# Kernel tuning notes

Hardware: AMD Instinct MI355X
Metric: run time of the kernel (lower is better)

The kernel has to match this reference:

```python
import jax, jax.numpy as jnp
import numpy as np

D = 512
DB = D // 4          # 128
R = 4                # window radius
KB = 9               # boundary kernel
DH = D // 2          # attn mlp hidden
VOCABS = {"quality": 64, "root": 13, "bass": 13, "key": 25}
COMPS = ["quality", "root", "bass", "key"]
B, T = 4, 4096


def _ln(x, g, b, eps=1e-5):
    mu = jnp.mean(x, axis=-1, keepdims=True)
    var = jnp.var(x, axis=-1, keepdims=True)
    return (x - mu) * jax.lax.rsqrt(var + eps) * g + b


def setup_inputs() -> dict:
    key = jax.random.key(0)
    ks = jax.random.split(key, 24)
    s = 0.02
    inp = {
        "h": jax.random.normal(ks[0], (B, T, D), jnp.float32),
        # boundary head
        "w_bnd": jax.random.normal(ks[1], (D,), jnp.float32) * s,
        "b_bnd": jnp.zeros((1,), jnp.float32),
        # boundary smoother conv1d(1,1,KB)
        "conv_k": jax.random.normal(ks[2], (KB,), jnp.float32) * s,
        "conv_b": jnp.zeros((1,), jnp.float32),
        # FiLM boundary embeddings
        "e0": jnp.zeros((DB,), jnp.float32),
        "e1": jax.random.normal(ks[3], (DB,), jnp.float32) * s,
        # LayerNorms
        "ln_in_g": jnp.ones((D + DB,), jnp.float32),
        "ln_in_b": jnp.zeros((D + DB,), jnp.float32),
        "ln_h_g": jnp.ones((D,), jnp.float32),
        "ln_h_b": jnp.zeros((D,), jnp.float32),
        # FiLM mlp
        "film_w": jax.random.normal(ks[4], (D + DB, 2 * D), jnp.float32) * s,
        "film_b": jnp.zeros((2 * D,), jnp.float32),
        # per-component attn MLP (stacked over 4 comps)
        "attn_w1": jax.random.normal(ks[5], (4, D, DH), jnp.float32) * s,
        "attn_b1": jnp.zeros((4, DH), jnp.float32),
        "attn_w2": jax.random.normal(ks[6], (4, DH), jnp.float32) * s,
        "attn_b2": jnp.zeros((4,), jnp.float32),
        # per-component projector first layer (stacked)
        "proj_w1": jax.random.normal(ks[7], (4, D, D), jnp.float32) * s,
        "proj_b1": jnp.zeros((4, D), jnp.float32),
    }
    for i, c in enumerate(COMPS):
        inp[f"proj_w2_{c[0]}" if c != "key" else "proj_w2_k"] = jax.random.normal(ks[8 + i], (D, VOCABS[c]), jnp.float32) * s
        inp[f"proj_b2_{c[0]}" if c != "key" else "proj_b2_k"] = jnp.zeros((VOCABS[c],), jnp.float32)
    return inp


def reference(h, w_bnd, b_bnd, conv_k, conv_b, e0, e1,
              ln_in_g, ln_in_b, ln_h_g, ln_h_b, film_w, film_b,
              attn_w1, attn_b1, attn_w2, attn_b2, proj_w1, proj_b1,
              proj_w2_q, proj_b2_q, proj_w2_r, proj_b2_r,
              proj_w2_b, proj_b2_b, proj_w2_k, proj_b2_k):
    Bz, Tz, Dz = h.shape
    # boundary head + smoothing (conv1d, same padding) + sigmoid
    bl = jnp.einsum("btd,d->bt", h, w_bnd) + b_bnd[0]            # [B,T]
    sm = jax.lax.conv_general_dilated(bl[:, None, :], conv_k[None, None, :],
                                      (1,), [(KB // 2, KB // 2)]) + conv_b[0]
    b_soft = jax.nn.sigmoid(sm[:, 0, :])                          # [B,T]
    # FiLM
    eb = b_soft[..., None] * e1 + (1.0 - b_soft[..., None]) * e0  # [B,T,DB]
    film_in = _ln(jnp.concatenate([h, eb], axis=-1), ln_in_g, ln_in_b)
    gb = film_in @ film_w + film_b                                # [B,T,2D]
    gamma, beta = gb[..., :Dz], gb[..., Dz:]
    z = _ln(h, ln_h_g, ln_h_b) * (1.0 + gamma) + beta             # [B,T,D]
    # local windows via replicate pad + gather
    hp = jnp.pad(h, ((0, 0), (R, R), (0, 0)), mode="edge")        # [B,T+2R,D]
    idx = jnp.arange(Tz)[:, None] + jnp.arange(2 * R + 1)[None, :]  # [T,W]
    local = hp[:, idx, :]                                         # [B,T,W,D]
    c = jnp.concatenate([z[:, :, None, :], local], axis=2)        # [B,T,C,D]
    # attention pooling for all 4 components at once
    s1 = jax.nn.gelu(jnp.einsum("btcd,kdh->kbtch", c, attn_w1)
                     + attn_b1[:, None, None, None, :], approximate=False)
    scores = jnp.einsum("kbtch,kh->kbtc", s1, attn_w2) + attn_b2[:, None, None, None]
    attn = jax.nn.softmax(scores, axis=-1)                        # [K,B,T,C]
    pooled = jnp.einsum("kbtc,btcd->kbtd", attn, c)               # [K,B,T,D]
    p1 = jax.nn.gelu(jnp.einsum("kbtd,kde->kbte", pooled, proj_w1)
                     + proj_b1[:, None, None, :], approximate=False)
    lq = p1[0] @ proj_w2_q + proj_b2_q
    lr = p1[1] @ proj_w2_r + proj_b2_r
    lb = p1[2] @ proj_w2_b + proj_b2_b
    lk = p1[3] @ proj_w2_k + proj_b2_k
    return jnp.concatenate([lq, lr, lb, lk, bl[..., None]], axis=-1)  # [B,T,116]
```

## Files before the change

kernel.cpp:

```cpp
#include <hip/hip_runtime.h>
#include <hip/hip_bf16.h>

typedef unsigned short u16;
typedef unsigned int u32;

#define NR 16384
#define TT 4096

typedef __bf16 bf16_t;
typedef bf16_t bf16x8 __attribute__((ext_vector_type(8)));
typedef float f32x4 __attribute__((ext_vector_type(4)));

__device__ __forceinline__ float b2f(u16 u){ return __uint_as_float(((u32)u)<<16); }
__device__ __forceinline__ u16 f2b(float f){
  u32 u = __float_as_uint(f);
  u32 r = u + 0x7fffu + ((u>>16)&1u);
  return (u16)(r>>16);
}
__device__ __forceinline__ void up2(u32 u, float&a, float&b){
  a = __uint_as_float(u<<16);
  b = __uint_as_float(u & 0xffff0000u);
}
__device__ __forceinline__ void ld8(const u16* p, float* f){
  uint4 v = *(const uint4*)p;
  up2(v.x,f[0],f[1]); up2(v.y,f[2],f[3]);
  up2(v.z,f[4],f[5]); up2(v.w,f[6],f[7]);
}
__device__ __forceinline__ float wred(float v){
  #pragma unroll
  for(int o=32;o>0;o>>=1) v += __shfl_down(v,o,64);
  return v;
}
__device__ __forceinline__ float gelu_f(float x){
  float x2 = x*x;
  float u = x*(0.7978845608f + 0.0356774081f*x2);
  float e = __expf(2.0f*u);
  float t = 1.0f - 2.0f*__builtin_amdgcn_rcpf(e+1.0f);
  return 0.5f*x*(1.0f+t);
}
__device__ __forceinline__ void gl_lds(const void* g, void* l){
  __builtin_amdgcn_global_load_lds(
      (__attribute__((address_space(1))) void*)(void*)g,
      (__attribute__((address_space(3))) void*)l, 16, 0, 0);
}

__global__ void k_tw(const float* __restrict__ src, u16* __restrict__ dst,
                     int K, int N, long long sS, long long sD){
  __shared__ float t[32][33];
  const float* S = src + (size_t)blockIdx.z*sS;
  u16* D = dst + (size_t)blockIdx.z*sD;
  int k0 = blockIdx.y*32, n0 = blockIdx.x*32;
  int r = threadIdx.x>>5, c = threadIdx.x&31;
  #pragma unroll
  for(int p=0;p<4;p++) t[r+p*8][c] = S[(size_t)(k0+r+p*8)*N + n0 + c];
  __syncthreads();
  #pragma unroll
  for(int p=0;p<4;p++) D[(size_t)(n0+r+p*8)*K + k0 + c] = f2b(t[c][r+p*8]);
}

__global__ void k_w2c(const float* __restrict__ wq, const float* __restrict__ bq,
                      const float* __restrict__ wr, const float* __restrict__ br,
                      const float* __restrict__ wb_, const float* __restrict__ bb_,
                      const float* __restrict__ wk, const float* __restrict__ bk,
                      u16* __restrict__ W2c, float* __restrict__ b2c){
  int idx = blockIdx.x;
  int p = idx>>5, j = idx&31, tid = threadIdx.x;
  const float* Wm; const float* Bm; int V; int cofs = 0;
  if(p<=1){ Wm=wq; Bm=bq; V=64; cofs = p*32; }
  else if(p==2){ Wm=wr; Bm=br; V=13; }
  else if(p==3){ Wm=wb_; Bm=bb_; V=13; }
  else { Wm=wk; Bm=bk; V=25; }
  int c = j + cofs;
  bool valid = c < V;
  for(int k=tid;k<512;k+=256)
    W2c[(size_t)idx*512 + k] = f2b(valid ? Wm[(size_t)k*V + c] : 0.f);
  if(tid==0) b2c[idx] = valid ? Bm[c] : 0.f;
}

__global__ void k_bnd(const float* __restrict__ h, const float* __restrict__ wb,
                      const float* __restrict__ bb,
                      float* __restrict__ bl, float* __restrict__ hsum, float* __restrict__ hss,
                      u16* __restrict__ hbf, float* __restrict__ out){
  int wave = threadIdx.x>>6, lane = threadIdx.x&63;
  int n = blockIdx.x*4 + wave;
  const float4* hp = (const float4*)(h + (size_t)n*512 + lane*8);
  const float4* wp = (const float4*)(wb + lane*8);
  float4 h0 = hp[0], h1 = hp[1], w0 = wp[0], w1 = wp[1];
  float hv[8] = {h0.x,h0.y,h0.z,h0.w,h1.x,h1.y,h1.z,h1.w};
  float wv[8] = {w0.x,w0.y,w0.z,w0.w,w1.x,w1.y,w1.z,w1.w};
  float dot=0.f, s=0.f, ss=0.f;
  #pragma unroll
  for(int i=0;i<8;i++){ dot += hv[i]*wv[i]; s += hv[i]; ss += hv[i]*hv[i]; }
  u16* hd = hbf + (size_t)n*512 + lane*8;
  *(ushort4*)hd     = make_ushort4(f2b(hv[0]),f2b(hv[1]),f2b(hv[2]),f2b(hv[3]));
  *(ushort4*)(hd+4) = make_ushort4(f2b(hv[4]),f2b(hv[5]),f2b(hv[6]),f2b(hv[7]));
  dot = wred(dot); s = wred(s); ss = wred(ss);
  if(lane==0){
    float v = dot + bb[0];
    bl[n] = v; hsum[n]=s; hss[n]=ss;
    out[(size_t)n*116 + 115] = v;
  }
}

__global__ void k_conv(const float* __restrict__ bl, const float* __restrict__ ck,
                       const float* __restrict__ cb, float* __restrict__ bsoft){
  int n = blockIdx.x*256 + threadIdx.x;
  int b = n>>12, t = n&4095;
  float acc = cb[0];
  #pragma unroll
  for(int i=0;i<9;i++){
    int tt = t-4+i;
    if(tt>=0 && tt<TT) acc += bl[(b<<12)+tt]*ck[i];
  }
  bsoft[n] = 1.0f/(1.0f+expf(-acc));
}

__global__ void k_filmin(const float* __restrict__ h, const float* __restrict__ bsoft,
                         const float* __restrict__ e0, const float* __restrict__ e1,
                         const float* __restrict__ g, const float* __restrict__ bb,
                         u16* __restrict__ fin){
  __shared__ float xb[640];
  __shared__ float red[8];
  int n = blockIdx.x, tid = threadIdx.x;
  float bs = bsoft[n];
  float s=0.f, ss=0.f;
  for(int idx=tid; idx<640; idx+=256){
    float v;
    if(idx<512) v = h[(size_t)n*512+idx];
    else { int j=idx-512; v = bs*e1[j] + (1.0f-bs)*e0[j]; }
    xb[idx]=v; s+=v; ss+=v*v;
  }
  s = wred(s); ss = wred(ss);
  int wave = tid>>6, lane = tid&63;
  if(lane==0){ red[wave]=s; red[wave+4]=ss; }
  __syncthreads();
  float S = red[0]+red[1]+red[2]+red[3];
  float SS = red[4]+red[5]+red[6]+red[7];
  float mu = S*(1.0f/640.0f);
  float var = SS*(1.0f/640.0f) - mu*mu;
  float rs = rsqrtf(var + 1e-5f);
  for(int idx=tid; idx<640; idx+=256){
    float v = (xb[idx]-mu)*rs*g[idx] + bb[idx];
    fin[(size_t)n*640+idx] = f2b(v);
  }
}

__global__ __launch_bounds__(256) void k_film(
    const u16* __restrict__ fin, const u16* __restrict__ WT, const float* __restrict__ fbias,
    const float* __restrict__ hsum, const float* __restrict__ hss,
    const float* __restrict__ lng, const float* __restrict__ lnb,
    const u16* __restrict__ hbf, u16* __restrict__ z){
  __shared__ __align__(16) u16 As[128*32];
  __shared__ __align__(16) u16 Bg[128*32];
  __shared__ __align__(16) u16 Bb2[128*32];
  int tid = threadIdx.x, wave = tid>>6, lane = tid&63;
  int cg0 = blockIdx.x*128, row0 = blockIdx.y*128;
  int wr = (wave>>1)*64, wc = (wave&1)*64;
  int lrow = lane>>2, lcol = (lane&3)*8, m15 = lane&15, q = lane>>4;
  f32x4 ag[4][4] = {}, ab[4][4] = {};
  for(int k0=0;k0<640;k0+=32){
    const u16* ga = fin + (size_t)(row0 + wave*32 + lrow)*640 + k0 + lcol;
    u16* la = As + wave*32*32;
    gl_lds(ga, la); gl_lds(ga + (size_t)16*640, la + 16*32);
    const u16* gg = WT + (size_t)(cg0 + wave*32 + lrow)*640 + k0 + lcol;
    u16* lg = Bg + wave*32*32;
    gl_lds(gg, lg); gl_lds(gg + (size_t)16*640, lg + 16*32);
    const u16* gb2 = WT + (size_t)(cg0 + 512 + wave*32 + lrow)*640 + k0 + lcol;
    u16* lb2 = Bb2 + wave*32*32;
    gl_lds(gb2, lb2); gl_lds(gb2 + (size_t)16*640, lb2 + 16*32);
    __syncthreads();
    bf16x8 af[4], bg[4], bb[4];
    #pragma unroll
    for(int i=0;i<4;i++){
      af[i] = *(const bf16x8*)&As[(wr + i*16 + m15)*32 + q*8];
      bg[i] = *(const bf16x8*)&Bg[(wc + i*16 + m15)*32 + q*8];
      bb[i] = *(const bf16x8*)&Bb2[(wc + i*16 + m15)*32 + q*8];
    }
    #pragma unroll
    for(int i=0;i<4;i++)
      #pragma unroll
      for(int j=0;j<4;j++){
        ag[i][j] = __builtin_amdgcn_mfma_f32_16x16x32_bf16(bg[j], af[i], ag[i][j], 0,0,0);
        ab[i][j] = __builtin_amdgcn_mfma_f32_16x16x32_bf16(bb[j], af[i], ab[i][j], 0,0,0);
      }
    __syncthreads();
  }
  #pragma unroll
  for(int i=0;i<4;i++){
    int m = row0 + wr + i*16 + m15;
    float mu = hsum[m]*(1.0f/512.0f);
    float var = hss[m]*(1.0f/512.0f) - mu*mu;
    float rs = rsqrtf(var + 1e-5f);
    #pragma unroll
    for(int j=0;j<4;j++){
      int d0 = cg0 + wc + j*16 + q*4;
      float4 g4 = *(const float4*)&lng[d0];
      float4 b4 = *(const float4*)&lnb[d0];
      float4 fg = *(const float4*)&fbias[d0];
      float4 fb = *(const float4*)&fbias[512+d0];
      float hv[4];
      { ushort4 hb4 = *(const ushort4*)(hbf + (size_t)m*512 + d0);
        hv[0]=b2f(hb4.x); hv[1]=b2f(hb4.y); hv[2]=b2f(hb4.z); hv[3]=b2f(hb4.w); }
      float gm[4] = {ag[i][j][0]+fg.x, ag[i][j][1]+fg.y, ag[i][j][2]+fg.z, ag[i][j][3]+fg.w};
      float bt[4] = {ab[i][j][0]+fb.x, ab[i][j][1]+fb.y, ab[i][j][2]+fb.z, ab[i][j][3]+fb.w};
      float gg4[4] = {g4.x,g4.y,g4.z,g4.w}, bb4[4] = {b4.x,b4.y,b4.z,b4.w};
      u16 o[4];
      #pragma unroll
      for(int r=0;r<4;r++){
        float ln = (hv[r]-mu)*rs*gg4[r] + bb4[r];
        o[r] = f2b(ln*(1.0f+gm[r]) + bt[r]);
      }
      *(ushort4*)(z + (size_t)m*512 + d0) = make_ushort4(o[0],o[1],o[2],o[3]);
    }
  }
}

__global__ __launch_bounds__(256) void k_msc(
    const u16* __restrict__ hb, const u16* __restrict__ zb,
    const u16* __restrict__ WT, const float* __restrict__ b1,
    const float* __restrict__ w2, float* __restrict__ sch, float* __restrict__ scz){
  __shared__ __align__(16) u16 As[64*32];
  __shared__ __align__(16) u16 Bs[256*32];
  int tid = threadIdx.x, wave = tid>>6, lane = tid&63;
  int bz = blockIdx.y, hk = bz>>1, src = bz&1;
  const u16* X = src ? zb : hb;
  float* sc = src ? scz : sch;
  int row0 = blockIdx.x*64;
  const u16* Wb = WT + (size_t)hk*256*512;
  int lrow = lane>>2, lcol = (lane&3)*8, m15 = lane&15, q = lane>>4;
  int wc = wave*64;
  f32x4 acc[4][4] = {};
  for(int k0=0;k0<512;k0+=32){
    gl_lds(X + (size_t)(row0 + wave*16 + lrow)*512 + k0 + lcol, As + wave*16*32);
    const u16* gw = Wb + (size_t)(wave*64 + lrow)*512 + k0 + lcol;
    u16* lb = Bs + wave*64*32;
    gl_lds(gw, lb);
    gl_lds(gw + (size_t)16*512, lb + 16*32);
    gl_lds(gw + (size_t)32*512, lb + 32*32);
    gl_lds(gw + (size_t)48*512, lb + 48*32);
    __syncthreads();
    bf16x8 af[4], bfr[4];
    #pragma unroll
    for(int i=0;i<4;i++){
      af[i]  = *(const bf16x8*)&As[(i*16 + m15)*32 + q*8];
      bfr[i] = *(const bf16x8*)&Bs[(wc + i*16 + m15)*32 + q*8];
    }
    #pragma unroll
    for(int i=0;i<4;i++)
      #pragma unroll
      for(int j=0;j<4;j++)
        acc[i][j] = __builtin_amdgcn_mfma_f32_16x16x32_bf16(bfr[j], af[i], acc[i][j], 0,0,0);
    __syncthreads();
  }
  #pragma unroll
  for(int i=0;i<4;i++){
    float part = 0.f;
    #pragma unroll
    for(int j=0;j<4;j++){
      int n0 = wc + j*16 + q*4;
      float4 bias = *(const float4*)&b1[hk*256 + n0];
      float4 wv   = *(const float4*)&w2[hk*256 + n0];
      part += gelu_f(acc[i][j][0]+bias.x)*wv.x;
      part += gelu_f(acc[i][j][1]+bias.y)*wv.y;
      part += gelu_f(acc[i][j][2]+bias.z)*wv.z;
      part += gelu_f(acc[i][j][3]+bias.w)*wv.w;
    }
    part += __shfl_xor(part, 16, 64);
    part += __shfl_xor(part, 32, 64);
    if(q==0) atomicAdd(&sc[(size_t)hk*NR + row0 + i*16 + m15], part);
  }
}

__global__ __launch_bounds__(256) void k_proj(
    const u16* __restrict__ P, const u16* __restrict__ WT, const float* __restrict__ Bv,
    u16* __restrict__ X2){
  __shared__ __align__(16) u16 As[64*32];
  __shared__ __align__(16) u16 Bs[256*32];
  int tid = threadIdx.x, wave = tid>>6, lane = tid&63;
  int hk = blockIdx.z;
  int row0 = blockIdx.y*64, col0 = blockIdx.x*256;
  const u16* Xb = P + (size_t)hk*NR*512;
  const u16* Wb = WT + (size_t)hk*512*512 + (size_t)col0*512;
  const float* Bq = Bv + hk*512;
  int lrow = lane>>2, lcol = (lane&3)*8, m15 = lane&15, q = lane>>4;
  int wc = wave*64;
  f32x4 acc[4][4] = {};
  for(int k0=0;k0<512;k0+=32){
    gl_lds(Xb + (size_t)(row0 + wave*16 + lrow)*512 + k0 + lcol, As + wave*16*32);
    const u16* gw = Wb + (size_t)(wave*64 + lrow)*512 + k0 + lcol;
    u16* lb = Bs + wave*64*32;
    gl_lds(gw, lb);
    gl_lds(gw + (size_t)16*512, lb + 16*32);
    gl_lds(gw + (size_t)32*512, lb + 32*32);
    gl_lds(gw + (size_t)48*512, lb + 48*32);
    __syncthreads();
    bf16x8 af[4], bfr[4];
    #pragma unroll
    for(int i=0;i<4;i++){
      af[i]  = *(const bf16x8*)&As[(i*16 + m15)*32 + q*8];
      bfr[i] = *(const bf16x8*)&Bs[(wc + i*16 + m15)*32 + q*8];
    }
    #pragma unroll
    for(int i=0;i<4;i++)
      #pragma unroll
      for(int j=0;j<4;j++)
        acc[i][j] = __builtin_amdgcn_mfma_f32_16x16x32_bf16(bfr[j], af[i], acc[i][j], 0,0,0);
    __syncthreads();
  }
  #pragma unroll
  for(int i=0;i<4;i++){
    size_t mrow = (size_t)(row0 + i*16 + m15)*2048 + hk*512;
    #pragma unroll
    for(int j=0;j<4;j++){
      int n0 = col0 + wc + j*16 + q*4;
      float4 bias = *(const float4*)&Bq[n0];
      float v0 = gelu_f(acc[i][j][0] + bias.x);
      float v1 = gelu_f(acc[i][j][1] + bias.y);
      float v2 = gelu_f(acc[i][j][2] + bias.z);
      float v3 = gelu_f(acc[i][j][3] + bias.w);
      *(ushort4*)(X2 + mrow + n0) = make_ushort4(f2b(v0),f2b(v1),f2b(v2),f2b(v3));
    }
  }
}

__global__ __launch_bounds__(256) void k_f2(
    const u16* __restrict__ X2, const u16* __restrict__ W2c, const float* __restrict__ b2c,
    float* __restrict__ out){
  __shared__ __align__(16) u16 As[128*32];
  __shared__ __align__(16) u16 Bs[32*32];
  int tid = threadIdx.x, wave = tid>>6, lane = tid&63;
  int row0 = blockIdx.x*128, p = blockIdx.y;
  int hk = (p<=1)?0:(p-1);
  int B0 = (p==0)?0:(p==1)?32:(p==2)?64:(p==3)?77:90;
  int V  = (p<=1)?32:(p==4)?25:13;
  int lrow = lane>>2, lcol = (lane&3)*8, m15 = lane&15, q = lane>>4;
  f32x4 acc[2][2] = {};
  for(int k0=0;k0<512;k0+=32){
    const u16* ga = X2 + (size_t)(row0 + wave*32 + lrow)*2048 + hk*512 + k0 + lcol;
    u16* la = As + wave*32*32;
    gl_lds(ga, la);
    gl_lds(ga + (size_t)16*2048, la + 16*32);
    if(wave<2){
      const u16* gw = W2c + (size_t)(p*32 + wave*16 + lrow)*512 + k0 + lcol;
      gl_lds(gw, Bs + wave*16*32);
    }
    __syncthreads();
    bf16x8 af[2], bfr[2];
    #pragma unroll
    for(int i=0;i<2;i++) af[i] = *(const bf16x8*)&As[(wave*32 + i*16 + m15)*32 + q*8];
    #pragma unroll
    for(int j=0;j<2;j++) bfr[j] = *(const bf16x8*)&Bs[(j*16+m15)*32 + q*8];
    #pragma unroll
    for(int i=0;i<2;i++)
      #pragma unroll
      for(int j=0;j<2;j++)
        acc[i][j] = __builtin_amdgcn_mfma_f32_16x16x32_bf16(bfr[j], af[i], acc[i][j], 0,0,0);
    __syncthreads();
  }
  #pragma unroll
  for(int i=0;i<2;i++){
    size_t mrow = (size_t)(row0 + wave*32 + i*16 + m15)*116;
    #pragma unroll
    for(int j=0;j<2;j++){
      int nl0 = j*16 + q*4;
      #pragma unroll
      for(int r=0;r<4;r++){
        int nl = nl0 + r;
        if(nl < V) out[mrow + B0 + nl] = acc[i][j][r] + b2c[p*32+nl];
      }
    }
  }
}

__global__ __launch_bounds__(256) void k_pool(
    const u16* __restrict__ hb, const u16* __restrict__ z,
    const float* __restrict__ sch, const float* __restrict__ scz,
    u16* __restrict__ P){
  int wave = threadIdx.x>>6, lane = threadIdx.x&63;
  int n = blockIdx.x*4 + wave;
  int b = n>>12, t = n&4095;
  int k = lane&3, j = lane>>2;
  float s;
  if(j==0) s = scz[(size_t)k*NR+n];
  else if(j<10){
    int tc = t-5+j; tc = tc<0?0:(tc>TT-1?TT-1:tc);
    s = sch[(size_t)k*NR + (b<<12) + tc];
  } else s = -1e30f;
  float m = s;
  #pragma unroll
  for(int o=4;o<64;o<<=1) m = fmaxf(m, __shfl_xor(m,o,64));
  float e = (j<10)? expf(s-m) : 0.f;
  float sum = e;
  #pragma unroll
  for(int o=4;o<64;o<<=1) sum += __shfl_xor(sum,o,64);
  float ev = e/sum;
  int d0 = lane*8;
  float acc[4][8] = {};
  #pragma unroll
  for(int jj=0;jj<10;jj++){
    const u16* src;
    if(jj==0) src = z + (size_t)n*512 + d0;
    else {
      int tc = t-5+jj; tc = tc<0?0:(tc>TT-1?TT-1:tc);
      src = hb + ((size_t)(b<<12)+tc)*512 + d0;
    }
    float f[8]; ld8(src, f);
    float w0 = __shfl(ev, jj*4+0, 64);
    float w1 = __shfl(ev, jj*4+1, 64);
    float w2 = __shfl(ev, jj*4+2, 64);
    float w3 = __shfl(ev, jj*4+3, 64);
    #pragma unroll
    for(int i=0;i<8;i++){
      acc[0][i] += w0*f[i];
      acc[1][i] += w1*f[i];
      acc[2][i] += w2*f[i];
      acc[3][i] += w3*f[i];
    }
  }
  #pragma unroll
  for(int kk=0;kk<4;kk++){
    u16* dst = P + ((size_t)kk*NR + n)*512 + d0;
    *(ushort4*)dst     = make_ushort4(f2b(acc[kk][0]),f2b(acc[kk][1]),f2b(acc[kk][2]),f2b(acc[kk][3]));
    *(ushort4*)(dst+4) = make_ushort4(f2b(acc[kk][4]),f2b(acc[kk][5]),f2b(acc[kk][6]),f2b(acc[kk][7]));
  }
}

#define OFF_BL     0u
#define OFF_BSOFT  65536u
#define OFF_HSUM   131072u
#define OFF_HSS    196608u
#define OFF_SCH    262144u
#define OFF_SCZ    524288u
#define OFF_FIN    786432u
#define OFF_Z      55312384u
#define OFF_HBF    72089600u
#define OFF_WF     88866816u
#define OFF_WA     90177536u
#define OFF_WP     91226112u
#define OFF_P      93323264u
#define OFF_W2C    160432128u
#define OFF_B2C    160595968u

extern "C" void kernel_launch(void* const* d_in, const int* in_sizes, int n_in,
                              void* d_out, int out_size, void* d_ws, size_t ws_size,
                              hipStream_t stream){
  const float* h       = (const float*)d_in[0];
  const float* w_bnd   = (const float*)d_in[1];
  const float* b_bnd   = (const float*)d_in[2];
  const float* conv_k  = (const float*)d_in[3];
  const float* conv_b  = (const float*)d_in[4];
  const float* e0      = (const float*)d_in[5];
  const float* e1      = (const float*)d_in[6];
  const float* ln_in_g = (const float*)d_in[7];
  const float* ln_in_b = (const float*)d_in[8];
  const float* ln_h_g  = (const float*)d_in[9];
  const float* ln_h_b  = (const float*)d_in[10];
  const float* film_w  = (const float*)d_in[11];
  const float* film_b  = (const float*)d_in[12];
  const float* attn_w1 = (const float*)d_in[13];
  const float* attn_b1 = (const float*)d_in[14];
  const float* attn_w2 = (const float*)d_in[15];
  const float* proj_w1 = (const float*)d_in[17];
  const float* proj_b1 = (const float*)d_in[18];
  const float* wq = (const float*)d_in[19];
  const float* bq = (const float*)d_in[20];
  const float* wr = (const float*)d_in[21];
  const float* br = (const float*)d_in[22];
  const float* wb_ = (const float*)d_in[23];
  const float* bb_ = (const float*)d_in[24];
  const float* wk = (const float*)d_in[25];
  const float* bk = (const float*)d_in[26];
  float* out = (float*)d_out;
  char* ws = (char*)d_ws;

  float* bl    = (float*)(ws + OFF_BL);
  float* bsoft = (float*)(ws + OFF_BSOFT);
  float* hsum  = (float*)(ws + OFF_HSUM);
  float* hss   = (float*)(ws + OFF_HSS);
  float* sch   = (float*)(ws + OFF_SCH);
  float* scz   = (float*)(ws + OFF_SCZ);
  u16* fin     = (u16*)(ws + OFF_FIN);
  u16* X2      = (u16*)(ws + OFF_FIN);
  u16* z       = (u16*)(ws + OFF_Z);
  u16* hbf     = (u16*)(ws + OFF_HBF);
  u16* wfilm   = (u16*)(ws + OFF_WF);
  u16* wattn   = (u16*)(ws + OFF_WA);
  u16* wproj   = (u16*)(ws + OFF_WP);
  u16* P       = (u16*)(ws + OFF_P);
  u16* w2c     = (u16*)(ws + OFF_W2C);
  float* b2c   = (float*)(ws + OFF_B2C);

  hipMemsetAsync(ws + OFF_SCH, 0, 524288, stream);

  {
    dim3 g(1024/32, 640/32, 1);
    k_tw<<<g,256,0,stream>>>(film_w, wfilm, 640, 1024, 0, 0);
  }
  {
    dim3 g(256/32, 512/32, 4);
    k_tw<<<g,256,0,stream>>>(attn_w1, wattn, 512, 256, 512LL*256, 256LL*512);
  }
  {
    dim3 g(512/32, 512/32, 4);
    k_tw<<<g,256,0,stream>>>(proj_w1, wproj, 512, 512, 512LL*512, 512LL*512);
  }
  k_w2c<<<160,256,0,stream>>>(wq,bq,wr,br,wb_,bb_,wk,bk, w2c, b2c);

  k_bnd<<<NR/4,256,0,stream>>>(h,w_bnd,b_bnd,bl,hsum,hss,hbf,out);
  k_conv<<<NR/256,256,0,stream>>>(bl,conv_k,conv_b,bsoft);
  k_filmin<<<NR,256,0,stream>>>(h,bsoft,e0,e1,ln_in_g,ln_in_b,fin);

  {
    dim3 g(4, NR/128);
    k_film<<<g,256,0,stream>>>(fin, wfilm, film_b, hsum, hss, ln_h_g, ln_h_b, hbf, z);
  }

  {
    dim3 g(NR/64, 8);
    k_msc<<<g,256,0,stream>>>(hbf, z, wattn, attn_b1, attn_w2, sch, scz);
  }

  k_pool<<<NR/4,256,0,stream>>>(hbf,z,sch,scz,P);

  {
    dim3 g(2, NR/64, 4);
    k_proj<<<g,256,0,stream>>>(P, wproj, proj_b1, X2);
  }

  {
    dim3 g(NR/128, 5);
    k_f2<<<g,256,0,stream>>>(X2, w2c, b2c, out);
  }
}
```

Measured before the change: 402.8 us.

## Reuse precomputed row stats in FiLM input LN and double K-step GEMM loops

The FiLM input LayerNorm no longer re-reads h in fp32 or reduces across the block. It computes the 640-wide mean and variance algebraically from the hsum/hss already produced by k_bnd plus precomputed sums of e0/e1, then reads h from the bf16 copy. Separately, every MFMA GEMM kernel now loads two 32-wide K slices per barrier pair, halving the number of __syncthreads and giving the loads more in flight, at the cost of double the LDS per block and possibly lower occupancy. Reading h from bf16 slightly changes numerics, and the variance is now a one-pass E[x^2]-mu^2 formula.

```diff
diff --git a/kernel.cpp b/kernel.cpp
--- a/kernel.cpp
+++ b/kernel.cpp
@@ -77,6 +77,17 @@
   if(tid==0) b2c[idx] = valid ? Bm[c] : 0.f;
 }
 
+__global__ void k_esum(const float* __restrict__ e0, const float* __restrict__ e1,
+                       float* __restrict__ es){
+  int lane = threadIdx.x & 63;
+  float x0 = e0[lane], x1 = e0[lane+64];
+  float y0 = e1[lane], y1 = e1[lane+64];
+  float s0 = x0+x1, s1 = y0+y1;
+  float q0 = x0*x0+x1*x1, q1 = y0*y0+y1*y1, c = x0*y0+x1*y1;
+  s0 = wred(s0); s1 = wred(s1); q0 = wred(q0); q1 = wred(q1); c = wred(c);
+  if(lane==0){ es[0]=s0; es[1]=s1; es[2]=q0; es[3]=q1; es[4]=c; }
+}
+
 __global__ void k_bnd(const float* __restrict__ h, const float* __restrict__ wb,
                       const float* __restrict__ bb,
                       float* __restrict__ bl, float* __restrict__ hsum, float* __restrict__ hss,
@@ -115,34 +126,36 @@
   bsoft[n] = 1.0f/(1.0f+expf(-acc));
 }
 
-__global__ void k_filmin(const float* __restrict__ h, const float* __restrict__ bsoft,
+__global__ void k_filmin(const u16* __restrict__ hbf, const float* __restrict__ bsoft,
                          const float* __restrict__ e0, const float* __restrict__ e1,
+                         const float* __restrict__ es,
+                         const float* __restrict__ hsum, const float* __restrict__ hss,
                          const float* __restrict__ g, const float* __restrict__ bb,
                          u16* __restrict__ fin){
-  __shared__ float xb[640];
-  __shared__ float red[8];
   int n = blockIdx.x, tid = threadIdx.x;
-  float bs = bsoft[n];
-  float s=0.f, ss=0.f;
-  for(int idx=tid; idx<640; idx+=256){
-    float v;
-    if(idx<512) v = h[(size_t)n*512+idx];
-    else { int j=idx-512; v = bs*e1[j] + (1.0f-bs)*e0[j]; }
-    xb[idx]=v; s+=v; ss+=v*v;
-  }
-  s = wred(s); ss = wred(ss);
-  int wave = tid>>6, lane = tid&63;
-  if(lane==0){ red[wave]=s; red[wave+4]=ss; }
-  __syncthreads();
-  float S = red[0]+red[1]+red[2]+red[3];
-  float SS = red[4]+red[5]+red[6]+red[7];
+  if(tid >= 160) return;
+  float bs = bsoft[n], os = 1.0f - bs;
+  float S  = hsum[n] + bs*es[1] + os*es[0];
+  float SS = hss[n] + bs*bs*es[3] + 2.0f*bs*os*es[4] + os*os*es[2];
   float mu = S*(1.0f/640.0f);
   float var = SS*(1.0f/640.0f) - mu*mu;
   float rs = rsqrtf(var + 1e-5f);
-  for(int idx=tid; idx<640; idx+=256){
-    float v = (xb[idx]-mu)*rs*g[idx] + bb[idx];
-    fin[(size_t)n*640+idx] = f2b(v);
-  }
+  int d = tid*4;
+  float v[4];
+  if(d < 512){
+    ushort4 hv = *(const ushort4*)(hbf + (size_t)n*512 + d);
+    v[0]=b2f(hv.x); v[1]=b2f(hv.y); v[2]=b2f(hv.z); v[3]=b2f(hv.w);
+  } else {
+    float4 a = *(const float4*)(e1 + d - 512);
+    float4 b0 = *(const float4*)(e0 + d - 512);
+    v[0]=bs*a.x+os*b0.x; v[1]=bs*a.y+os*b0.y; v[2]=bs*a.z+os*b0.z; v[3]=bs*a.w+os*b0.w;
+  }
+  float4 g4 = *(const float4*)(g + d);
+  float4 b4 = *(const float4*)(bb + d);
+  u16 o[4];
+  o[0]=f2b((v[0]-mu)*rs*g4.x+b4.x); o[1]=f2b((v[1]-mu)*rs*g4.y+b4.y);
+  o[2]=f2b((v[2]-mu)*rs*g4.z+b4.z); o[3]=f2b((v[3]-mu)*rs*g4.w+b4.w);
+  *(ushort4*)(fin + (size_t)n*640 + d) = make_ushort4(o[0],o[1],o[2],o[3]);
 }
 
 __global__ __launch_bounds__(256) void k_film(
@@ -150,39 +163,46 @@
     const float* __restrict__ hsum, const float* __restrict__ hss,
     const float* __restrict__ lng, const float* __restrict__ lnb,
     const u16* __restrict__ hbf, u16* __restrict__ z){
-  __shared__ __align__(16) u16 As[128*32];
-  __shared__ __align__(16) u16 Bg[128*32];
-  __shared__ __align__(16) u16 Bb2[128*32];
+  __shared__ __align__(16) u16 As[2][128*32];
+  __shared__ __align__(16) u16 Bg[2][128*32];
+  __shared__ __align__(16) u16 Bb2[2][128*32];
   int tid = threadIdx.x, wave = tid>>6, lane = tid&63;
   int cg0 = blockIdx.x*128, row0 = blockIdx.y*128;
   int wr = (wave>>1)*64, wc = (wave&1)*64;
   int lrow = lane>>2, lcol = (lane&3)*8, m15 = lane&15, q = lane>>4;
   f32x4 ag[4][4] = {}, ab[4][4] = {};
-  for(int k0=0;k0<640;k0+=32){
-    const u16* ga = fin + (size_t)(row0 + wave*32 + lrow)*640 + k0 + lcol;
-    u16* la = As + wave*32*32;
-    gl_lds(ga, la); gl_lds(ga + (size_t)16*640, la + 16*32);
-    const u16* gg = WT + (size_t)(cg0 + wave*32 + lrow)*640 + k0 + lcol;
-    u16* lg = Bg + wave*32*32;
-    gl_lds(gg, lg); gl_lds(gg + (size_t)16*640, lg + 16*32);
-    const u16* gb2 = WT + (size_t)(cg0 + 512 + wave*32 + lrow)*640 + k0 + lcol;
-    u16* lb2 = Bb2 + wave*32*32;
-    gl_lds(gb2, lb2); gl_lds(gb2 + (size_t)16*640, lb2 + 16*32);
-    __syncthreads();
-    bf16x8 af[4], bg[4], bb[4];
-    #pragma unroll
-    for(int i=0;i<4;i++){
-      af[i] = *(const bf16x8*)&As[(wr + i*16 + m15)*32 + q*8];
-      bg[i] = *(const bf16x8*)&Bg[(wc + i*16 + m15)*32 + q*8];
-      bb[i] = *(const bf16x8*)&Bb2[(wc + i*16 + m15)*32 + q*8];
-    }
-    #pragma unroll
-    for(int i=0;i<4;i++)
-      #pragma unroll
-      for(int j=0;j<4;j++){
-        ag[i][j] = __builtin_amdgcn_mfma_f32_16x16x32_bf16(bg[j], af[i], ag[i][j], 0,0,0);
-        ab[i][j] = __builtin_amdgcn_mfma_f32_16x16x32_bf16(bb[j], af[i], ab[i][j], 0,0,0);
+  for(int k0=0;k0<640;k0+=64){
+    #pragma unroll
+    for(int hh=0;hh<2;hh++){
+      int kk = k0 + hh*32;
+      const u16* ga = fin + (size_t)(row0 + wave*32 + lrow)*640 + kk + lcol;
+      u16* la = &As[hh][wave*32*32];
+      gl_lds(ga, la); gl_lds(ga + (size_t)16*640, la + 16*32);
+      const u16* gg = WT + (size_t)(cg0 + wave*32 + lrow)*640 + kk + lcol;
+      u16* lg = &Bg[hh][wave*32*32];
+      gl_lds(gg, lg); gl_lds(gg + (size_t)16*640, lg + 16*32);
+      const u16* gb2 = WT + (size_t)(cg0 + 512 + wave*32 + lrow)*640 + kk + lcol;
+      u16* lb2 = &Bb2[hh][wave*32*32];
+      gl_lds(gb2, lb2); gl_lds(gb2 + (size_t)16*640, lb2 + 16*32);
+    }
+    __syncthreads();
+    #pragma unroll
+    for(int hh=0;hh<2;hh++){
+      bf16x8 af[4], bg[4], bb[4];
+      #pragma unroll
+      for(int i=0;i<4;i++){
+        af[i] = *(const bf16x8*)&As[hh][(wr + i*16 + m15)*32 + q*8];
+        bg[i] = *(const bf16x8*)&Bg[hh][(wc + i*16 + m15)*32 + q*8];
+        bb[i] = *(const bf16x8*)&Bb2[hh][(wc + i*16 + m15)*32 + q*8];
       }
+      #pragma unroll
+      for(int i=0;i<4;i++)
+        #pragma unroll
+        for(int j=0;j<4;j++){
+          ag[i][j] = __builtin_amdgcn_mfma_f32_16x16x32_bf16(bg[j], af[i], ag[i][j], 0,0,0);
+          ab[i][j] = __builtin_amdgcn_mfma_f32_16x16x32_bf16(bb[j], af[i], ab[i][j], 0,0,0);
+        }
+    }
     __syncthreads();
   }
   #pragma unroll
@@ -219,8 +239,8 @@
     const u16* __restrict__ hb, const u16* __restrict__ zb,
     const u16* __restrict__ WT, const float* __restrict__ b1,
     const float* __restrict__ w2, float* __restrict__ sch, float* __restrict__ scz){
-  __shared__ __align__(16) u16 As[64*32];
-  __shared__ __align__(16) u16 Bs[256*32];
+  __shared__ __align__(16) u16 As[2][64*32];
+  __shared__ __align__(16) u16 Bs[2][256*32];
   int tid = threadIdx.x, wave = tid>>6, lane = tid&63;
   int bz = blockIdx.y, hk = bz>>1, src = bz&1;
   const u16* X = src ? zb : hb;
@@ -230,26 +250,31 @@
   int lrow = lane>>2, lcol = (lane&3)*8, m15 = lane&15, q = lane>>4;
   int wc = wave*64;
   f32x4 acc[4][4] = {};
-  for(int k0=0;k0<512;k0+=32){
-    gl_lds(X + (size_t)(row0 + wave*16 + lrow)*512 + k0 + lcol, As + wave*16*32);
-    const u16* gw = Wb + (size_t)(wave*64 + lrow)*512 + k0 + lcol;
-    u16* lb = Bs + wave*64*32;
-    gl_lds(gw, lb);
-    gl_lds(gw + (size_t)16*512, lb + 16*32);
-    gl_lds(gw + (size_t)32*512, lb + 32*32);
-    gl_lds(gw + (size_t)48*512, lb + 48*32);
-    __syncthreads();
-    bf16x8 af[4], bfr[4];
-    #pragma unroll
-    for(int i=0;i<4;i++){
-      af[i]  = *(const bf16x8*)&As[(i*16 + m15)*32 + q*8];
-      bfr[i] = *(const bf16x8*)&Bs[(wc + i*16 + m15)*32 + q*8];
-    }
-    #pragma unroll
-    for(int i=0;i<4;i++)
-      #pragma unroll
-      for(int j=0;j<4;j++)
-        acc[i][j] = __builtin_amdgcn_mfma_f32_16x16x32_bf16(bfr[j], af[i], acc[i][j], 0,0,0);
+  for(int k0=0;k0<512;k0+=64){
+    #pragma unroll
+    for(int hh=0;hh<2;hh++){
+      int kk = k0 + hh*32;
+      gl_lds(X + (size_t)(row0 + wave*16 + lrow)*512 + kk + lcol, &As[hh][wave*16*32]);
+      #pragma unroll
+      for(int r=0;r<4;r++)
+        gl_lds(Wb + (size_t)(wave*64 + r*16 + lrow)*512 + kk + lcol,
+               &Bs[hh][(wave*64 + r*16)*32]);
+    }
+    __syncthreads();
+    #pragma unroll
+    for(int hh=0;hh<2;hh++){
+      bf16x8 af[4], bfr[4];
+      #pragma unroll
+      for(int i=0;i<4;i++){
+        af[i]  = *(const bf16x8*)&As[hh][(i*16 + m15)*32 + q*8];
+        bfr[i] = *(const bf16x8*)&Bs[hh][(wc + i*16 + m15)*32 + q*8];
+      }
+      #pragma unroll
+      for(int i=0;i<4;i++)
+        #pragma unroll
+        for(int j=0;j<4;j++)
+          acc[i][j] = __builtin_amdgcn_mfma_f32_16x16x32_bf16(bfr[j], af[i], acc[i][j], 0,0,0);
+    }
     __syncthreads();
   }
   #pragma unroll
@@ -274,8 +299,8 @@
 __global__ __launch_bounds__(256) void k_proj(
     const u16* __restrict__ P, const u16* __restrict__ WT, const float* __restrict__ Bv,
     u16* __restrict__ X2){
-  __shared__ __align__(16) u16 As[64*32];
-  __shared__ __align__(16) u16 Bs[256*32];
+  __shared__ __align__(16) u16 As[2][64*32];
+  __shared__ __align__(16) u16 Bs[2][256*32];
   int tid = threadIdx.x, wave = tid>>6, lane = tid&63;
   int hk = blockIdx.z;
   int row0 = blockIdx.y*64, col0 = blockIdx.x*256;
@@ -285,26 +310,31 @@
   int lrow = lane>>2, lcol = (lane&3)*8, m15 = lane&15, q = lane>>4;
   int wc = wave*64;
   f32x4 acc[4][4] = {};
-  for(int k0=0;k0<512;k0+=32){
-    gl_lds(Xb + (size_t)(row0 + wave*16 + lrow)*512 + k0 + lcol, As + wave*16*32);
-    const u16* gw = Wb + (size_t)(wave*64 + lrow)*512 + k0 + lcol;
-    u16* lb = Bs + wave*64*32;
-    gl_lds(gw, lb);
-    gl_lds(gw + (size_t)16*512, lb + 16*32);
-    gl_lds(gw + (size_t)32*512, lb + 32*32);
-    gl_lds(gw + (size_t)48*512, lb + 48*32);
-    __syncthreads();
-    bf16x8 af[4], bfr[4];
-    #pragma unroll
-    for(int i=0;i<4;i++){
-      af[i]  = *(const bf16x8*)&As[(i*16 + m15)*32 + q*8];
-      bfr[i] = *(const bf16x8*)&Bs[(wc + i*16 + m15)*32 + q*8];
-    }
-    #pragma unroll
-    for(int i=0;i<4;i++)
-      #pragma unroll
-      for(int j=0;j<4;j++)
-        acc[i][j] = __builtin_amdgcn_mfma_f32_16x16x32_bf16(bfr[j], af[i], acc[i][j], 0,0,0);
+  for(int k0=0;k0<512;k0+=64){
+    #pragma unroll
+    for(int hh=0;hh<2;hh++){
+      int kk = k0 + hh*32;
+      gl_lds(Xb + (size_t)(row0 + wave*16 + lrow)*512 + kk + lcol, &As[hh][wave*16*32]);
+      #pragma unroll
+      for(int r=0;r<4;r++)
+        gl_lds(Wb + (size_t)(wave*64 + r*16 + lrow)*512 + kk + lcol,
+               &Bs[hh][(wave*64 + r*16)*32]);
+    }
+    __syncthreads();
+    #pragma unroll
+    for(int hh=0;hh<2;hh++){
+      bf16x8 af[4], bfr[4];
+      #pragma unroll
+      for(int i=0;i<4;i++){
+        af[i]  = *(const bf16x8*)&As[hh][(i*16 + m15)*32 + q*8];
+        bfr[i] = *(const bf16x8*)&Bs[hh][(wc + i*16 + m15)*32 + q*8];
+      }
+      #pragma unroll
+      for(int i=0;i<4;i++)
+        #pragma unroll
+        for(int j=0;j<4;j++)
+          acc[i][j] = __builtin_amdgcn_mfma_f32_16x16x32_bf16(bfr[j], af[i], acc[i][j], 0,0,0);
+    }
     __syncthreads();
   }
   #pragma unroll
@@ -326,8 +356,8 @@
 __global__ __launch_bounds__(256) void k_f2(
     const u16* __restrict__ X2, const u16* __restrict__ W2c, const float* __restrict__ b2c,
     float* __restrict__ out){
-  __shared__ __align__(16) u16 As[128*32];
-  __shared__ __align__(16) u16 Bs[32*32];
+  __shared__ __align__(16) u16 As[2][128*32];
+  __shared__ __align__(16) u16 Bs[2][32*32];
   int tid = threadIdx.x, wave = tid>>6, lane = tid&63;
   int row0 = blockIdx.x*128, p = blockIdx.y;
   int hk = (p<=1)?0:(p-1);
@@ -335,26 +365,31 @@
   int V  = (p<=1)?32:(p==4)?25:13;
   int lrow = lane>>2, lcol = (lane&3)*8, m15 = lane&15, q = lane>>4;
   f32x4 acc[2][2] = {};
-  for(int k0=0;k0<512;k0+=32){
-    const u16* ga = X2 + (size_t)(row0 + wave*32 + lrow)*2048 + hk*512 + k0 + lcol;
-    u16* la = As + wave*32*32;
-    gl_lds(ga, la);
-    gl_lds(ga + (size_t)16*2048, la + 16*32);
-    if(wave<2){
-      const u16* gw = W2c + (size_t)(p*32 + wave*16 + lrow)*512 + k0 + lcol;
-      gl_lds(gw, Bs + wave*16*32);
-    }
-    __syncthreads();
-    bf16x8 af[2], bfr[2];
-    #pragma unroll
-    for(int i=0;i<2;i++) af[i] = *(const bf16x8*)&As[(wave*32 + i*16 + m15)*32 + q*8];
-    #pragma unroll
-    for(int j=0;j<2;j++) bfr[j] = *(const bf16x8*)&Bs[(j*16+m15)*32 + q*8];
-    #pragma unroll
-    for(int i=0;i<2;i++)
-      #pragma unroll
-      for(int j=0;j<2;j++)
-        acc[i][j] = __builtin_amdgcn_mfma_f32_16x16x32_bf16(bfr[j], af[i], acc[i][j], 0,0,0);
+  for(int k0=0;k0<512;k0+=64){
+    #pragma unroll
+    for(int hh=0;hh<2;hh++){
+      int kk = k0 + hh*32;
+      const u16* ga = X2 + (size_t)(row0 + wave*32 + lrow)*2048 + hk*512 + kk + lcol;
+      u16* la = &As[hh][wave*32*32];
+      gl_lds(ga, la);
+      gl_lds(ga + (size_t)16*2048, la + 16*32);
+      if(wave<2)
+        gl_lds(W2c + (size_t)(p*32 + wave*16 + lrow)*512 + kk + lcol, &Bs[hh][wave*16*32]);
+    }
+    __syncthreads();
+    #pragma unroll
+    for(int hh=0;hh<2;hh++){
+      bf16x8 af[2], bfr[2];
+      #pragma unroll
+      for(int i=0;i<2;i++) af[i] = *(const bf16x8*)&As[hh][(wave*32 + i*16 + m15)*32 + q*8];
+      #pragma unroll
+      for(int j=0;j<2;j++) bfr[j] = *(const bf16x8*)&Bs[hh][(j*16+m15)*32 + q*8];
+      #pragma unroll
+      for(int i=0;i<2;i++)
+        #pragma unroll
+        for(int j=0;j<2;j++)
+          acc[i][j] = __builtin_amdgcn_mfma_f32_16x16x32_bf16(bfr[j], af[i], acc[i][j], 0,0,0);
+    }
     __syncthreads();
   }
   #pragma unroll
@@ -440,6 +475,7 @@
 #define OFF_P      93323264u
 #define OFF_W2C    160432128u
 #define OFF_B2C    160595968u
+#define OFF_ES     160596608u
 
 extern "C" void kernel_launch(void* const* d_in, const int* in_sizes, int n_in,
                               void* d_out, int out_size, void* d_ws, size_t ws_size,
@@ -489,6 +525,7 @@
   u16* P       = (u16*)(ws + OFF_P);
   u16* w2c     = (u16*)(ws + OFF_W2C);
   float* b2c   = (float*)(ws + OFF_B2C);
+  float* es    = (float*)(ws + OFF_ES);
 
   hipMemsetAsync(ws + OFF_SCH, 0, 524288, stream);
 
@@ -505,10 +542,11 @@
     k_tw<<<g,256,0,stream>>>(proj_w1, wproj, 512, 512, 512LL*512, 512LL*512);
   }
   k_w2c<<<160,256,0,stream>>>(wq,bq,wr,br,wb_,bb_,wk,bk, w2c, b2c);
+  k_esum<<<1,64,0,stream>>>(e0, e1, es);
 
   k_bnd<<<NR/4,256,0,stream>>>(h,w_bnd,b_bnd,bl,hsum,hss,hbf,out);
   k_conv<<<NR/256,256,0,stream>>>(bl,conv_k,conv_b,bsoft);
-  k_filmin<<<NR,256,0,stream>>>(h,bsoft,e0,e1,ln_in_g,ln_in_b,fin);
+  k_filmin<<<NR,256,0,stream>>>(hbf,bsoft,e0,e1,es,hsum,hss,ln_in_g,ln_in_b,fin);
 
   {
     dim3 g(4, NR/128);
```

After: 387.5 us. 1.04x faster.
